# Kernel tuning notes

Hardware: AMD Instinct MI355X
Metric: run time of the kernel (lower is better)

The kernel has to match this reference:

```python
import jax, jax.numpy as jnp
import numpy as np

B, S, HID = 1, 2048, 2048
NH, NKV, HD = 32, 8, 64
INTER = 8192
EPS = 1e-6


def rmsnorm(x, w, eps=EPS):
    xf = x.astype(jnp.float32)
    inv = jax.lax.rsqrt(jnp.mean(xf * xf, axis=-1, keepdims=True) + eps)
    return (xf * inv * w).astype(x.dtype)


def rope(x, sin_t, cos_t):
    # x: [B, S, H, D]; sin/cos: [S, D//2]
    sin = sin_t[None, :, None, :]
    cos = cos_t[None, :, None, :]
    d2 = x.shape[-1] // 2
    x0, x1 = x[..., :d2], x[..., d2:]
    return jnp.concatenate((x0 * cos - x1 * sin, x0 * sin + x1 * cos), axis=-1)


def setup_inputs() -> dict:
    key = jax.random.key(0)
    ks = jax.random.split(key, 12)
    hidden_states = jax.random.normal(ks[0], (B, S, HID), dtype=jnp.float32)
    # realistic RoPE tables
    inv_freq = 1.0 / (10000.0 ** (np.arange(0, HD // 2, dtype=np.float32) * 2.0 / HD))
    ang = np.arange(S, dtype=np.float32)[:, None] * inv_freq[None, :]
    sin_table = jnp.asarray(np.sin(ang))
    cos_table = jnp.asarray(np.cos(ang))
    s = 0.02
    return {
        "hidden_states": hidden_states,
        "sin_table": sin_table,
        "cos_table": cos_table,
        "ln1_w": jnp.ones((HID,), jnp.float32),
        "ln2_w": jnp.ones((HID,), jnp.float32),
        "wq": jax.random.normal(ks[1], (HID, NH * HD), jnp.float32) * s,
        "wk": jax.random.normal(ks[2], (HID, NKV * HD), jnp.float32) * s,
        "wv": jax.random.normal(ks[3], (HID, NKV * HD), jnp.float32) * s,
        "wo": jax.random.normal(ks[4], (NH * HD, HID), jnp.float32) * s,
        "w_gate": jax.random.normal(ks[5], (HID, INTER), jnp.float32) * s,
        "w_up": jax.random.normal(ks[6], (HID, INTER), jnp.float32) * s,
        "w_down": jax.random.normal(ks[7], (INTER, HID), jnp.float32) * s,
    }


def attention(x, sin_t, cos_t, wq, wk, wv, wo):
    b, s, _ = x.shape
    q = (x @ wq).reshape(b, s, NH, HD)
    k = (x @ wk).reshape(b, s, NKV, HD)
    v = (x @ wv).reshape(b, s, NKV, HD).transpose(0, 2, 1, 3)  # [B,Hk,S,D]
    q = rope(q, sin_t, cos_t).transpose(0, 2, 1, 3)  # [B,Hq,S,D]
    k = rope(k, sin_t, cos_t).transpose(0, 2, 1, 3)  # [B,Hk,S,D]
    g = NH // NKV
    k = jnp.repeat(k, g, axis=1)
    v = jnp.repeat(v, g, axis=1)
    scale = 1.0 / np.sqrt(HD)
    scores = jnp.einsum("bhqd,bhkd->bhqk", q, k) * scale
    mask = jnp.tril(jnp.ones((s, s), dtype=bool))
    scores = jnp.where(mask, scores, -jnp.inf)
    probs = jax.nn.softmax(scores, axis=-1)
    out = jnp.einsum("bhqk,bhkd->bhqd", probs, v)
    out = out.transpose(0, 2, 1, 3).reshape(b, s, NH * HD)
    return out @ wo


def reference(hidden_states, sin_table, cos_table, ln1_w, ln2_w, wq, wk, wv, wo, w_gate, w_up, w_down):
    x = hidden_states
    x = x + attention(rmsnorm(x, ln1_w), sin_table, cos_table, wq, wk, wv, wo)
    h = rmsnorm(x, ln2_w)
    x = x + (jax.nn.silu(h @ w_gate) * (h @ w_up)) @ w_down
    return x
```

## Files before the change

kernel.cpp:

```cpp
#include <hip/hip_runtime.h>
#include <hip/hip_bf16.h>

typedef float f32x4 __attribute__((ext_vector_type(4)));
typedef unsigned int u32x4 __attribute__((ext_vector_type(4)));
typedef _Float16 f16x4 __attribute__((ext_vector_type(4)));
typedef unsigned short u16;

#define S_LEN 2048
#define HID 2048
#define NHEAD 32
#define NKVH 8
#define HDIM 64

__device__ __forceinline__ unsigned short f2bf_bits(float f) {
    unsigned int u = __builtin_bit_cast(unsigned int, f);
    unsigned int r = u + 0x7fffu + ((u >> 16) & 1u);
    return (unsigned short)(r >> 16);
}
__device__ __forceinline__ float bf2f(unsigned short b) {
    unsigned int u = ((unsigned int)b) << 16;
    return __builtin_bit_cast(float, u);
}

__device__ __forceinline__ f32x4 mfma_bf16(u32x4 a, u32x4 b, f32x4 c) {
    asm("v_mfma_f32_16x16x32_bf16 %0, %1, %2, %0" : "+v"(c) : "v"(a), "v"(b));
    return c;
}

__device__ __forceinline__ void gload_lds16(const void* g, void* l) {
    __builtin_amdgcn_global_load_lds(
        (const __attribute__((address_space(1))) void*)g,
        (__attribute__((address_space(3))) void*)l, 16, 0, 0);
}

__global__ __launch_bounds__(256)
void rmsnorm_k(const float* __restrict__ x, const float* __restrict__ wgt,
               unsigned short* __restrict__ out)
{
    int row = blockIdx.x;
    int t = threadIdx.x;
    const float* xr = x + (size_t)row * HID;
    f32x4 a = *(const f32x4*)(xr + t * 8);
    f32x4 b = *(const f32x4*)(xr + t * 8 + 4);
    float s = 0.f;
#pragma unroll
    for (int i = 0; i < 4; ++i) s += a[i] * a[i] + b[i] * b[i];
#pragma unroll
    for (int off = 32; off > 0; off >>= 1) s += __shfl_down(s, off);
    __shared__ float red[4];
    if ((t & 63) == 0) red[t >> 6] = s;
    __syncthreads();
    float tot = red[0] + red[1] + red[2] + red[3];
    float inv = rsqrtf(tot * (1.0f / (float)HID) + 1e-6f);
    f32x4 wa = *(const f32x4*)(wgt + t * 8);
    f32x4 wb = *(const f32x4*)(wgt + t * 8 + 4);
    unsigned int pk[4];
#pragma unroll
    for (int i = 0; i < 2; ++i) {
        pk[i]     = (unsigned)f2bf_bits(a[2*i] * inv * wa[2*i]) |
                    ((unsigned)f2bf_bits(a[2*i+1] * inv * wa[2*i+1]) << 16);
        pk[i + 2] = (unsigned)f2bf_bits(b[2*i] * inv * wb[2*i]) |
                    ((unsigned)f2bf_bits(b[2*i+1] * inv * wb[2*i+1]) << 16);
    }
    u32x4 ov; ov[0] = pk[0]; ov[1] = pk[1]; ov[2] = pk[2]; ov[3] = pk[3];
    *(u32x4*)(out + (size_t)row * HID + t * 8) = ov;
}

__global__ __launch_bounds__(256)
void transpose_cvt(const float* __restrict__ in, unsigned short* __restrict__ out,
                   int K, int N)
{
    __shared__ unsigned short tile[64 * 65];
    int kb = blockIdx.y * 64, nb = blockIdx.x * 64;
    int t = threadIdx.x;
    int r = t >> 2, c0 = (t & 3) * 16;
    const float* src = in + (size_t)(kb + r) * N + nb + c0;
#pragma unroll
    for (int j = 0; j < 4; ++j) {
        f32x4 v = *(const f32x4*)(src + j * 4);
#pragma unroll
        for (int i = 0; i < 4; ++i)
            tile[r * 65 + c0 + j * 4 + i] = f2bf_bits(v[i]);
    }
    __syncthreads();
    unsigned short e[16];
#pragma unroll
    for (int j = 0; j < 16; ++j) e[j] = tile[(c0 + j) * 65 + r];
    u32x4 o0, o1;
#pragma unroll
    for (int j = 0; j < 4; ++j) {
        o0[j] = (unsigned)e[2*j] | ((unsigned)e[2*j+1] << 16);
        o1[j] = (unsigned)e[8 + 2*j] | ((unsigned)e[8 + 2*j+1] << 16);
    }
    unsigned short* dst = out + (size_t)(nb + r) * K + kb + c0;
    *(u32x4*)(dst) = o0;
    *(u32x4*)(dst + 8) = o1;
}

__global__ __launch_bounds__(256)
void rope_k(unsigned short* __restrict__ qkv, const float* __restrict__ sin_t,
            const float* __restrict__ cos_t)
{
    int s = blockIdx.x;
    for (int it = threadIdx.x; it < (NHEAD + NKVH) * 32; it += 256) {
        int slot = it >> 5;
        int d = it & 31;
        int col = (slot < NHEAD) ? slot * 64 + d : HID + (slot - NHEAD) * 64 + d;
        unsigned short* p = qkv + (size_t)s * 3072 + col;
        float x0 = bf2f(p[0]);
        float x1 = bf2f(p[32]);
        float c = cos_t[s * 32 + d];
        float sn = sin_t[s * 32 + d];
        p[0]  = f2bf_bits(x0 * c - x1 * sn);
        p[32] = f2bf_bits(x0 * sn + x1 * c);
    }
}

__global__ __launch_bounds__(256)
void transpose_v(const unsigned short* __restrict__ qkv, unsigned short* __restrict__ vT)
{
    __shared__ unsigned short tile[64][80];
    int kb = blockIdx.x * 64, kvh = blockIdx.y;
    int t = threadIdx.x;
    int r = t >> 2, c0 = (t & 3) * 16;
    const unsigned short* src = qkv + (size_t)(kb + r) * 3072 + 2560 + kvh * 64 + c0;
    u32x4 v0 = *(const u32x4*)(src);
    u32x4 v1 = *(const u32x4*)(src + 8);
    *(u32x4*)&tile[r][c0] = v0;
    *(u32x4*)&tile[r][c0 + 8] = v1;
    __syncthreads();
    int d = t >> 2, k0 = (t & 3) * 16;
    unsigned short e[16];
#pragma unroll
    for (int j = 0; j < 16; ++j) e[j] = tile[k0 + j][d];
    u32x4 o0, o1;
#pragma unroll
    for (int j = 0; j < 4; ++j) {
        o0[j] = (unsigned)e[2*j] | ((unsigned)e[2*j+1] << 16);
        o1[j] = (unsigned)e[8 + 2*j] | ((unsigned)e[8 + 2*j+1] << 16);
    }
    int s0 = ((k0 >> 3) ^ (d & 7)) & 7;
    int s1 = (((k0 >> 3) + 1) ^ (d & 7)) & 7;
    unsigned short* dst = vT + ((size_t)kvh * 64 + d) * 2048 + kb;
    *(u32x4*)(dst + s0 * 8) = o0;
    *(u32x4*)(dst + s1 * 8) = o1;
}

template <int EPI>
__global__ __launch_bounds__(256)
void gemm_bt(const unsigned short* __restrict__ A,
             const unsigned short* __restrict__ Bt,
             void* __restrict__ outp, const void* __restrict__ auxp,
             int M, int N, int Kc, int lda)
{
    __shared__ unsigned short As[2][128 * 32];
    __shared__ unsigned short Bs[2][128 * 32];
    int t = threadIdx.x, w = t >> 6, l = t & 63;
    int rb = blockIdx.y, cb = blockIdx.x, zb = blockIdx.z;
    int wr = w >> 1, wc = w & 1;
    int l4 = l >> 4, l15 = l & 15;
    int arow = l >> 2, acol = (l & 3) * 8;
    f32x4 acc[4][4] = {};
    const unsigned short* Ag = A + (size_t)rb * 128 * lda + (size_t)zb * Kc
                                 + (size_t)(w * 16 + arow) * lda + acol;
    const unsigned short* Bg = Bt + (size_t)cb * 128 * lda + (size_t)zb * Kc
                                 + (size_t)(w * 16 + arow) * lda + acol;
    int nk = Kc >> 5;

#define STAGE(buf, kt)                                                          \
    {                                                                           \
        const unsigned short* Agk = Ag + (size_t)(kt) * 32;                     \
        const unsigned short* Bgk = Bg + (size_t)(kt) * 32;                     \
        gload_lds16(Agk, &As[buf][w * 512]);                                    \
        gload_lds16(Agk + (size_t)64 * lda, &As[buf][(4 + w) * 512]);           \
        gload_lds16(Bgk, &Bs[buf][w * 512]);                                    \
        gload_lds16(Bgk + (size_t)64 * lda, &Bs[buf][(4 + w) * 512]);           \
    }

    STAGE(0, 0);
    __syncthreads();
    int cur = 0;
    for (int kt = 0; kt < nk; ++kt) {
        if (kt + 1 < nk) STAGE(cur ^ 1, kt + 1);
        u32x4 af[4], bfr[4];
#pragma unroll
        for (int i = 0; i < 4; ++i)
            af[i] = *(const u32x4*)(&As[cur][(wr * 64 + i * 16 + l15) * 32 + l4 * 8]);
#pragma unroll
        for (int n = 0; n < 4; ++n)
            bfr[n] = *(const u32x4*)(&Bs[cur][(wc * 64 + n * 16 + l15) * 32 + l4 * 8]);
#pragma unroll
        for (int i = 0; i < 4; ++i)
#pragma unroll
            for (int n = 0; n < 4; ++n)
                acc[i][n] = mfma_bf16(af[i], bfr[n], acc[i][n]);
        __syncthreads();
        cur ^= 1;
    }
#undef STAGE

    int row0 = rb * 128 + wr * 64 + l4 * 4;
    int col0 = cb * 128 + wc * 64 + l15;
#pragma unroll
    for (int i = 0; i < 4; ++i) {
#pragma unroll
        for (int n = 0; n < 4; ++n) {
#pragma unroll
            for (int r = 0; r < 4; ++r) {
                int row = row0 + i * 16 + r;
                int col = col0 + n * 16;
                size_t idx = (size_t)row * N + col;
                float v = acc[i][n][r];
                if (EPI == 0) {
                    ((unsigned short*)outp)[idx] = f2bf_bits(v);
                } else if (EPI == 3) {
                    ((float*)outp)[idx] = v + ((const float*)auxp)[idx];
                } else {
                    ((_Float16*)outp)[(size_t)zb * M * N + idx] = (_Float16)v;
                }
            }
        }
    }
}

template <int KK, int QUAD, int WAITN>
__device__ __forceinline__ void phase8(u16* lds, int cur, f32x4 (&acc)[8][4],
                                       u32x4 (&bfv)[4],
                                       int aoff, int boff,
                                       const u16* Asrc, const u16* Bsrc,
                                       int K, int kt_next, bool dostage,
                                       int dst0, int dst1)
{
    const u16* ah = lds + (cur * 4 + KK * 2) * 8192 + aoff + QUAD * 2048;
    u32x4 af[4];
#pragma unroll
    for (int mi = 0; mi < 4; ++mi) af[mi] = *(const u32x4*)(ah + mi * 512);
    if (QUAD == 0) {
        const u16* bh = lds + (cur * 4 + KK * 2 + 1) * 8192 + boff;
#pragma unroll
        for (int ni = 0; ni < 4; ++ni) bfv[ni] = *(const u32x4*)(bh + ni * 512);
    }
    if (dostage) {
        const u16* src = (QUAD ? Bsrc : Asrc) + (size_t)kt_next * 64 + KK * 32;
        u16* d = lds + ((cur ^ 1) * 4 + (KK * 2 + QUAD)) * 8192;
        gload_lds16(src, d + dst0);
        gload_lds16(src + (size_t)128 * K, d + dst1);
    }
    __builtin_amdgcn_s_barrier();
    asm volatile("s_waitcnt lgkmcnt(0)" ::: "memory");
    __builtin_amdgcn_sched_barrier(0);
    __builtin_amdgcn_s_setprio(1);
#pragma unroll
    for (int mi = 0; mi < 4; ++mi)
#pragma unroll
        for (int ni = 0; ni < 4; ++ni)
            acc[QUAD * 4 + mi][ni] = mfma_bf16(af[mi], bfv[ni], acc[QUAD * 4 + mi][ni]);
    __builtin_amdgcn_s_setprio(0);
    if (WAITN == 4) asm volatile("s_waitcnt vmcnt(4)" ::: "memory");
    else if (WAITN == 0) asm volatile("s_waitcnt vmcnt(0)" ::: "memory");
    __builtin_amdgcn_s_barrier();
}

template <int EPI>
__global__ __launch_bounds__(512, 2)
void gemm8p(const u16* __restrict__ A, const u16* __restrict__ Bt,
            void* __restrict__ outp, const void* __restrict__ auxp,
            int M, int N, int K)
{
    extern __shared__ u16 lds[];
    const int tid = threadIdx.x;
    const int w = tid >> 6, l = tid & 63;
    const int wm = w >> 2, wn = w & 3;
    const int l4 = l >> 4, l15 = l & 15;

    int wg = blockIdx.x, nwg = gridDim.x;
    int swzb = ((nwg & 7) == 0) ? ((wg & 7) * (nwg >> 3) + (wg >> 3)) : wg;
    int rbs = M >> 8;
    int rb = swzb % rbs, cb = swzb / rbs;

    const int sw = ((tid & 3) ^ ((tid >> 3) & 3)) * 8;
    const int srow = tid >> 2;
    const u16* Asrc = A + (size_t)(rb * 256 + srow) * K + sw;
    const u16* Bsrc = Bt + (size_t)(cb * 256 + srow) * K + sw;
    const int dst0 = tid * 8, dst1 = (512 + tid) * 8;

    const int rswz = (l15 >> 1) & 3;
    const int aoff = (wm * 128 + l15) * 32 + (l4 ^ rswz) * 8;
    const int boff = (wn * 64 + l15) * 32 + (l4 ^ rswz) * 8;

    f32x4 acc[8][4] = {};
    u32x4 bfv[4];
    const int NT = K >> 6;

#pragma unroll
    for (int h = 0; h < 2; ++h) {
        const u16* sA = Asrc + h * 32;
        const u16* sB = Bsrc + h * 32;
        gload_lds16(sA, lds + (h * 2) * 8192 + dst0);
        gload_lds16(sA + (size_t)128 * K, lds + (h * 2) * 8192 + dst1);
        gload_lds16(sB, lds + (h * 2 + 1) * 8192 + dst0);
        gload_lds16(sB + (size_t)128 * K, lds + (h * 2 + 1) * 8192 + dst1);
    }
    asm volatile("s_waitcnt vmcnt(4)" ::: "memory");
    __builtin_amdgcn_s_barrier();

    for (int t = 0; t < NT - 1; ++t) {
        int cur = t & 1;
        phase8<0, 0, -1>(lds, cur, acc, bfv, aoff, boff, Asrc, Bsrc, K, t + 1, true, dst0, dst1);
        phase8<0, 1,  4>(lds, cur, acc, bfv, aoff, boff, Asrc, Bsrc, K, t + 1, true, dst0, dst1);
        phase8<1, 0, -1>(lds, cur, acc, bfv, aoff, boff, Asrc, Bsrc, K, t + 1, true, dst0, dst1);
        phase8<1, 1,  4>(lds, cur, acc, bfv, aoff, boff, Asrc, Bsrc, K, t + 1, true, dst0, dst1);
    }
    {
        int cur = (NT - 1) & 1;
        phase8<0, 0, -1>(lds, cur, acc, bfv, aoff, boff, Asrc, Bsrc, K, 0, false, dst0, dst1);
        phase8<0, 1,  0>(lds, cur, acc, bfv, aoff, boff, Asrc, Bsrc, K, 0, false, dst0, dst1);
        phase8<1, 0, -1>(lds, cur, acc, bfv, aoff, boff, Asrc, Bsrc, K, 0, false, dst0, dst1);
        phase8<1, 1, -1>(lds, cur, acc, bfv, aoff, boff, Asrc, Bsrc, K, 0, false, dst0, dst1);
    }

    int row0 = rb * 256 + wm * 128 + l4 * 4;
    int col0 = cb * 256 + wn * 64 + l15;
#pragma unroll
    for (int mi = 0; mi < 8; ++mi) {
#pragma unroll
        for (int ni = 0; ni < 4; ++ni) {
#pragma unroll
            for (int r = 0; r < 4; ++r) {
                int row = row0 + mi * 16 + r;
                int col = col0 + ni * 16;
                size_t idx = (size_t)row * N + col;
                float v = acc[mi][ni][r];
                if (EPI == 1) {
                    float sv = v / (1.0f + __expf(-v));
                    ((unsigned short*)outp)[idx] = f2bf_bits(sv);
                } else {
                    float gv = bf2f(((const unsigned short*)auxp)[idx]);
                    ((unsigned short*)outp)[idx] = f2bf_bits(v * gv);
                }
            }
        }
    }
}

__global__ __launch_bounds__(256)
void reduce_add4(float* __restrict__ out, const _Float16* __restrict__ p, int n)
{
    int i = (blockIdx.x * 256 + threadIdx.x) * 4;
    f32x4 a = *(const f32x4*)(out + i);
#pragma unroll
    for (int z = 0; z < 4; ++z) {
        f16x4 h = *(const f16x4*)(p + (size_t)z * n + i);
#pragma unroll
        for (int j = 0; j < 4; ++j) a[j] += (float)h[j];
    }
    *(f32x4*)(out + i) = a;
}

__global__ __launch_bounds__(256)
void attn_fwd(const unsigned short* __restrict__ qkv,
              const unsigned short* __restrict__ vT,
              unsigned short* __restrict__ out)
{
    int p = blockIdx.x, h = blockIdx.y, kvh = h >> 2;
    int t = threadIdx.x, w = t >> 6, l = t & 63;
    int l4 = l >> 4, l15 = l & 15;
    __shared__ unsigned short Ks[2][64 * 64];
    __shared__ unsigned short Vs[2][64 * 64];
    __shared__ unsigned short Pl[4][16 * 72];
    unsigned short* Pw = &Pl[w][0];

    const unsigned short* Kg = qkv + HID + kvh * 64;
    const unsigned short* Vg = vT + (size_t)kvh * 64 * 2048;

    int ch0 = w * 2, ch1 = w * 2 + 1;
    int rsub = l >> 3;
    int ksw = ((l & 7) ^ (rsub & 7)) * 8;
    int vcol = (l & 7) * 8;
    int sw0 = (l4 ^ (l15 & 7)) * 8;
    int sw1 = ((l4 | 4) ^ (l15 & 7)) * 8;

#define STAGE_KV(buf, kt)                                                         \
    {                                                                             \
        gload_lds16(Kg + (size_t)((kt) * 64 + ch0 * 8 + rsub) * 3072 + ksw,       \
                    &Ks[buf][ch0 * 512]);                                         \
        gload_lds16(Kg + (size_t)((kt) * 64 + ch1 * 8 + rsub) * 3072 + ksw,       \
                    &Ks[buf][ch1 * 512]);                                         \
        gload_lds16(Vg + (size_t)(ch0 * 8 + rsub) * 2048 + (kt) * 64 + vcol,      \
                    &Vs[buf][ch0 * 512]);                                         \
        gload_lds16(Vg + (size_t)(ch1 * 8 + rsub) * 2048 + (kt) * 64 + vcol,      \
                    &Vs[buf][ch1 * 512]);                                         \
    }

    const float SC2 = 0.18033688f;
    const float THR = 44.36f;
    const float BIG = -3.0e38f;

    for (int half = 0; half < 2; ++half) {
        int qb = half ? (31 - p) : p;
        int qrow0 = qb * 64 + w * 16;
        STAGE_KV(0, 0);
        const unsigned short* qg = qkv + (size_t)(qrow0 + l15) * 3072 + h * 64 + l4 * 8;
        u32x4 aq0 = *(const u32x4*)(qg);
        u32x4 aq1 = *(const u32x4*)(qg + 32);
        f32x4 o[4] = {};
        float m[4], ls[4] = {};
#pragma unroll
        for (int r = 0; r < 4; ++r) m[r] = BIG;
        __syncthreads();
        int cur = 0;
        for (int kt = 0; kt <= qb; ++kt) {
            if (kt < qb) STAGE_KV(cur ^ 1, kt + 1);
            f32x4 sc[4];
#pragma unroll
            for (int n = 0; n < 4; ++n) {
                const unsigned short* kb_ = &Ks[cur][(n * 16 + l15) * 64];
                u32x4 b0 = *(const u32x4*)(kb_ + sw0);
                u32x4 b1 = *(const u32x4*)(kb_ + sw1);
                f32x4 z = {};
                z = mfma_bf16(aq0, b0, z);
                z = mfma_bf16(aq1, b1, z);
                sc[n] = z;
            }
            if (kt == qb) {
#pragma unroll
                for (int n = 0; n < 4; ++n) {
                    int kcol = n * 16 + l15;
#pragma unroll
                    for (int r = 0; r < 4; ++r) {
                        int qr = w * 16 + l4 * 4 + r;
                        if (kcol > qr) sc[n][r] = BIG;
                    }
                }
            }
            float rmax[4];
#pragma unroll
            for (int r = 0; r < 4; ++r)
                rmax[r] = fmaxf(fmaxf(sc[0][r], sc[1][r]), fmaxf(sc[2][r], sc[3][r]));
#pragma unroll
            for (int msk = 1; msk <= 8; msk <<= 1)
#pragma unroll
                for (int r = 0; r < 4; ++r)
                    rmax[r] = fmaxf(rmax[r], __shfl_xor(rmax[r], msk));
            float need = 0.f;
#pragma unroll
            for (int r = 0; r < 4; ++r) need = fmaxf(need, rmax[r] - m[r]);
            if (__ballot(need > THR)) {
#pragma unroll
                for (int r = 0; r < 4; ++r) {
                    float mn = fmaxf(m[r], rmax[r]);
                    float al = __builtin_exp2f((m[r] - mn) * SC2);
                    m[r] = mn;
                    ls[r] *= al;
#pragma unroll
                    for (int nd = 0; nd < 4; ++nd) o[nd][r] *= al;
                }
            }
            float rs[4] = {}, ms[4];
#pragma unroll
            for (int r = 0; r < 4; ++r) ms[r] = m[r] * SC2;
#pragma unroll
            for (int n = 0; n < 4; ++n)
#pragma unroll
                for (int r = 0; r < 4; ++r) {
                    float pe = __builtin_exp2f(__builtin_fmaf(sc[n][r], SC2, -ms[r]));
                    sc[n][r] = pe;
                    rs[r] += pe;
                }
#pragma unroll
            for (int msk = 1; msk <= 8; msk <<= 1)
#pragma unroll
                for (int r = 0; r < 4; ++r) rs[r] += __shfl_xor(rs[r], msk);
#pragma unroll
            for (int r = 0; r < 4; ++r) ls[r] += rs[r];
#pragma unroll
            for (int n = 0; n < 4; ++n)
#pragma unroll
                for (int r = 0; r < 4; ++r)
                    Pw[(l4 * 4 + r) * 72 + n * 16 + l15] = f2bf_bits(sc[n][r]);
            asm volatile("s_waitcnt lgkmcnt(0)" ::: "memory");
            __builtin_amdgcn_sched_barrier(0);
            u32x4 ap0 = *(const u32x4*)(Pw + l15 * 72 + l4 * 8);
            u32x4 ap1 = *(const u32x4*)(Pw + l15 * 72 + 32 + l4 * 8);
#pragma unroll
            for (int nd = 0; nd < 4; ++nd) {
                const unsigned short* vb = &Vs[cur][(nd * 16 + l15) * 64];
                u32x4 bv0 = *(const u32x4*)(vb + sw0);
                u32x4 bv1 = *(const u32x4*)(vb + sw1);
                o[nd] = mfma_bf16(ap0, bv0, o[nd]);
                o[nd] = mfma_bf16(ap1, bv1, o[nd]);
            }
            __syncthreads();
            cur ^= 1;
        }
#undef STAGE_KV
        float linv[4];
#pragma unroll
        for (int r = 0; r < 4; ++r) linv[r] = 1.0f / ls[r];
#pragma unroll
        for (int nd = 0; nd < 4; ++nd)
#pragma unroll
            for (int r = 0; r < 4; ++r)
                out[(size_t)(qrow0 + l4 * 4 + r) * HID + h * 64 + nd * 16 + l15] =
                    f2bf_bits(o[nd][r] * linv[r]);
    }
}

extern "C" void kernel_launch(void* const* d_in, const int* in_sizes, int n_in,
                              void* d_out, int out_size, void* d_ws, size_t ws_size,
                              hipStream_t stream)
{
    const float* x     = (const float*)d_in[0];
    const float* sin_t = (const float*)d_in[1];
    const float* cos_t = (const float*)d_in[2];
    const float* ln1w  = (const float*)d_in[3];
    const float* ln2w  = (const float*)d_in[4];
    const float* wq    = (const float*)d_in[5];
    const float* wk    = (const float*)d_in[6];
    const float* wv    = (const float*)d_in[7];
    const float* wo    = (const float*)d_in[8];
    const float* wg    = (const float*)d_in[9];
    const float* wu    = (const float*)d_in[10];
    const float* wd    = (const float*)d_in[11];
    float* out = (float*)d_out;

    char* ws = (char*)d_ws;
    if (ws_size < 113246208u) return;
    unsigned short* wT   = (unsigned short*)(ws);
    unsigned short* xn   = (unsigned short*)(ws + 33554432u);
    unsigned short* qkv  = (unsigned short*)(ws + 41943040u);
    unsigned short* attn = (unsigned short*)(ws + 54525952u);
    unsigned short* vT   = (unsigned short*)(ws + 62914560u);
    _Float16*       part = (_Float16*)(ws + 33554432u);
    unsigned short* g    = (unsigned short*)(ws + 79691776u);

    hipFuncSetAttribute(reinterpret_cast<const void*>(&gemm8p<1>),
                        hipFuncAttributeMaxDynamicSharedMemorySize, 131072);
    hipFuncSetAttribute(reinterpret_cast<const void*>(&gemm8p<2>),
                        hipFuncAttributeMaxDynamicSharedMemorySize, 131072);

    rmsnorm_k<<<S_LEN, 256, 0, stream>>>(x, ln1w, xn);

    transpose_cvt<<<dim3(32, 32), 256, 0, stream>>>(wq, wT, 2048, 2048);
    transpose_cvt<<<dim3(8, 32), 256, 0, stream>>>(wk, wT + (size_t)2048 * 2048, 2048, 512);
    transpose_cvt<<<dim3(8, 32), 256, 0, stream>>>(wv, wT + (size_t)2560 * 2048, 2048, 512);

    gemm_bt<0><<<dim3(24, 16, 1), 256, 0, stream>>>(xn, wT, qkv, nullptr, 2048, 3072, 2048, 2048);

    rope_k<<<S_LEN, 256, 0, stream>>>(qkv, sin_t, cos_t);
    transpose_v<<<dim3(32, 8), 256, 0, stream>>>(qkv, vT);

    attn_fwd<<<dim3(16, 32), 256, 0, stream>>>(qkv, vT, attn);

    transpose_cvt<<<dim3(32, 32), 256, 0, stream>>>(wo, wT, 2048, 2048);
    gemm_bt<3><<<dim3(16, 16, 1), 256, 0, stream>>>(attn, wT, out, x, 2048, 2048, 2048, 2048);

    rmsnorm_k<<<S_LEN, 256, 0, stream>>>(out, ln2w, xn);

    transpose_cvt<<<dim3(128, 32), 256, 0, stream>>>(wg, wT, 2048, 8192);
    gemm8p<1><<<dim3(256), 512, 131072, stream>>>(xn, wT, g, nullptr, 2048, 8192, 2048);

    transpose_cvt<<<dim3(128, 32), 256, 0, stream>>>(wu, wT, 2048, 8192);
    gemm8p<2><<<dim3(256), 512, 131072, stream>>>(xn, wT, g, g, 2048, 8192, 2048);

    transpose_cvt<<<dim3(32, 128), 256, 0, stream>>>(wd, wT, 8192, 2048);
    gemm_bt<5><<<dim3(16, 16, 4), 256, 0, stream>>>(g, wT, part, nullptr, 2048, 2048, 2048, 8192);

    reduce_add4<<<4096, 256, 0, stream>>>(out, part, 4194304);
}
```

Baseline: 485.2 us.

## Use split-K 256x256 gemm8p for down-proj and split-K the o-proj

Extends the pipelined 256x256 gemm8p kernel with split-K support: a separate leading dimension, a K-chunk offset taken from blockIdx.y, and an fp16 partial-output epilogue. The down projection now runs on gemm8p (64 tiles x 4 K-splits) in place of the smaller-tile gemm_bt, aiming at higher MFMA efficiency. The o-projection is split into two K halves writing fp16 partials, followed by a new reduce kernel that adds the residual, so the grid has more blocks. The cost is an extra reduction kernel and fp16 rounding of the partial sums.

```diff
diff --git a/kernel.cpp b/kernel.cpp
--- a/kernel.cpp
+++ b/kernel.cpp
@@ -228,7 +228,7 @@
                                        u32x4 (&bfv)[4],
                                        int aoff, int boff,
                                        const u16* Asrc, const u16* Bsrc,
-                                       int K, int kt_next, bool dostage,
+                                       int lda, int kt_next, bool dostage,
                                        int dst0, int dst1)
 {
     const u16* ah = lds + (cur * 4 + KK * 2) * 8192 + aoff + QUAD * 2048;
@@ -244,7 +244,7 @@
         const u16* src = (QUAD ? Bsrc : Asrc) + (size_t)kt_next * 64 + KK * 32;
         u16* d = lds + ((cur ^ 1) * 4 + (KK * 2 + QUAD)) * 8192;
         gload_lds16(src, d + dst0);
-        gload_lds16(src + (size_t)128 * K, d + dst1);
+        gload_lds16(src + (size_t)128 * lda, d + dst1);
     }
     __builtin_amdgcn_s_barrier();
     asm volatile("s_waitcnt lgkmcnt(0)" ::: "memory");
@@ -265,13 +265,14 @@
 __global__ __launch_bounds__(512, 2)
 void gemm8p(const u16* __restrict__ A, const u16* __restrict__ Bt,
             void* __restrict__ outp, const void* __restrict__ auxp,
-            int M, int N, int K)
+            int M, int N, int Kc, int lda)
 {
     extern __shared__ u16 lds[];
     const int tid = threadIdx.x;
     const int w = tid >> 6, l = tid & 63;
     const int wm = w >> 2, wn = w & 3;
     const int l4 = l >> 4, l15 = l & 15;
+    const int zb = blockIdx.y;
 
     int wg = blockIdx.x, nwg = gridDim.x;
     int swzb = ((nwg & 7) == 0) ? ((wg & 7) * (nwg >> 3) + (wg >> 3)) : wg;
@@ -280,8 +281,8 @@
 
     const int sw = ((tid & 3) ^ ((tid >> 3) & 3)) * 8;
     const int srow = tid >> 2;
-    const u16* Asrc = A + (size_t)(rb * 256 + srow) * K + sw;
-    const u16* Bsrc = Bt + (size_t)(cb * 256 + srow) * K + sw;
+    const u16* Asrc = A + (size_t)(rb * 256 + srow) * lda + (size_t)zb * Kc + sw;
+    const u16* Bsrc = Bt + (size_t)(cb * 256 + srow) * lda + (size_t)zb * Kc + sw;
     const int dst0 = tid * 8, dst1 = (512 + tid) * 8;
 
     const int rswz = (l15 >> 1) & 3;
@@ -290,33 +291,33 @@
 
     f32x4 acc[8][4] = {};
     u32x4 bfv[4];
-    const int NT = K >> 6;
+    const int NT = Kc >> 6;
 
 #pragma unroll
     for (int h = 0; h < 2; ++h) {
         const u16* sA = Asrc + h * 32;
         const u16* sB = Bsrc + h * 32;
         gload_lds16(sA, lds + (h * 2) * 8192 + dst0);
-        gload_lds16(sA + (size_t)128 * K, lds + (h * 2) * 8192 + dst1);
+        gload_lds16(sA + (size_t)128 * lda, lds + (h * 2) * 8192 + dst1);
         gload_lds16(sB, lds + (h * 2 + 1) * 8192 + dst0);
-        gload_lds16(sB + (size_t)128 * K, lds + (h * 2 + 1) * 8192 + dst1);
+        gload_lds16(sB + (size_t)128 * lda, lds + (h * 2 + 1) * 8192 + dst1);
     }
     asm volatile("s_waitcnt vmcnt(4)" ::: "memory");
     __builtin_amdgcn_s_barrier();
 
     for (int t = 0; t < NT - 1; ++t) {
         int cur = t & 1;
-        phase8<0, 0, -1>(lds, cur, acc, bfv, aoff, boff, Asrc, Bsrc, K, t + 1, true, dst0, dst1);
-        phase8<0, 1,  4>(lds, cur, acc, bfv, aoff, boff, Asrc, Bsrc, K, t + 1, true, dst0, dst1);
-        phase8<1, 0, -1>(lds, cur, acc, bfv, aoff, boff, Asrc, Bsrc, K, t + 1, true, dst0, dst1);
-        phase8<1, 1,  4>(lds, cur, acc, bfv, aoff, boff, Asrc, Bsrc, K, t + 1, true, dst0, dst1);
+        phase8<0, 0, -1>(lds, cur, acc, bfv, aoff, boff, Asrc, Bsrc, lda, t + 1, true, dst0, dst1);
+        phase8<0, 1,  4>(lds, cur, acc, bfv, aoff, boff, Asrc, Bsrc, lda, t + 1, true, dst0, dst1);
+        phase8<1, 0, -1>(lds, cur, acc, bfv, aoff, boff, Asrc, Bsrc, lda, t + 1, true, dst0, dst1);
+        phase8<1, 1,  4>(lds, cur, acc, bfv, aoff, boff, Asrc, Bsrc, lda, t + 1, true, dst0, dst1);
     }
     {
         int cur = (NT - 1) & 1;
-        phase8<0, 0, -1>(lds, cur, acc, bfv, aoff, boff, Asrc, Bsrc, K, 0, false, dst0, dst1);
-        phase8<0, 1,  0>(lds, cur, acc, bfv, aoff, boff, Asrc, Bsrc, K, 0, false, dst0, dst1);
-        phase8<1, 0, -1>(lds, cur, acc, bfv, aoff, boff, Asrc, Bsrc, K, 0, false, dst0, dst1);
-        phase8<1, 1, -1>(lds, cur, acc, bfv, aoff, boff, Asrc, Bsrc, K, 0, false, dst0, dst1);
+        phase8<0, 0, -1>(lds, cur, acc, bfv, aoff, boff, Asrc, Bsrc, lda, 0, false, dst0, dst1);
+        phase8<0, 1,  0>(lds, cur, acc, bfv, aoff, boff, Asrc, Bsrc, lda, 0, false, dst0, dst1);
+        phase8<1, 0, -1>(lds, cur, acc, bfv, aoff, boff, Asrc, Bsrc, lda, 0, false, dst0, dst1);
+        phase8<1, 1, -1>(lds, cur, acc, bfv, aoff, boff, Asrc, Bsrc, lda, 0, false, dst0, dst1);
     }
 
     int row0 = rb * 256 + wm * 128 + l4 * 4;
@@ -334,9 +335,11 @@
                 if (EPI == 1) {
                     float sv = v / (1.0f + __expf(-v));
                     ((unsigned short*)outp)[idx] = f2bf_bits(sv);
-                } else {
+                } else if (EPI == 2) {
                     float gv = bf2f(((const unsigned short*)auxp)[idx]);
                     ((unsigned short*)outp)[idx] = f2bf_bits(v * gv);
+                } else {
+                    ((_Float16*)outp)[(size_t)zb * M * N + idx] = (_Float16)v;
                 }
             }
         }
@@ -350,6 +353,21 @@
     f32x4 a = *(const f32x4*)(out + i);
 #pragma unroll
     for (int z = 0; z < 4; ++z) {
+        f16x4 h = *(const f16x4*)(p + (size_t)z * n + i);
+#pragma unroll
+        for (int j = 0; j < 4; ++j) a[j] += (float)h[j];
+    }
+    *(f32x4*)(out + i) = a;
+}
+
+__global__ __launch_bounds__(256)
+void reduce_res2(float* __restrict__ out, const float* __restrict__ x,
+                 const _Float16* __restrict__ p, int n)
+{
+    int i = (blockIdx.x * 256 + threadIdx.x) * 4;
+    f32x4 a = *(const f32x4*)(x + i);
+#pragma unroll
+    for (int z = 0; z < 2; ++z) {
         f16x4 h = *(const f16x4*)(p + (size_t)z * n + i);
 #pragma unroll
         for (int j = 0; j < 4; ++j) a[j] += (float)h[j];
@@ -533,11 +551,14 @@
     unsigned short* vT   = (unsigned short*)(ws + 62914560u);
     _Float16*       part = (_Float16*)(ws + 33554432u);
     unsigned short* g    = (unsigned short*)(ws + 79691776u);
+    _Float16*       opart = (_Float16*)(ws + 79691776u);
 
     hipFuncSetAttribute(reinterpret_cast<const void*>(&gemm8p<1>),
                         hipFuncAttributeMaxDynamicSharedMemorySize, 131072);
     hipFuncSetAttribute(reinterpret_cast<const void*>(&gemm8p<2>),
                         hipFuncAttributeMaxDynamicSharedMemorySize, 131072);
+    hipFuncSetAttribute(reinterpret_cast<const void*>(&gemm8p<5>),
+                        hipFuncAttributeMaxDynamicSharedMemorySize, 131072);
 
     rmsnorm_k<<<S_LEN, 256, 0, stream>>>(x, ln1w, xn);
 
@@ -553,18 +574,19 @@
     attn_fwd<<<dim3(16, 32), 256, 0, stream>>>(qkv, vT, attn);
 
     transpose_cvt<<<dim3(32, 32), 256, 0, stream>>>(wo, wT, 2048, 2048);
-    gemm_bt<3><<<dim3(16, 16, 1), 256, 0, stream>>>(attn, wT, out, x, 2048, 2048, 2048, 2048);
+    gemm_bt<5><<<dim3(16, 16, 2), 256, 0, stream>>>(attn, wT, opart, nullptr, 2048, 2048, 1024, 2048);
+    reduce_res2<<<4096, 256, 0, stream>>>(out, x, opart, 4194304);
 
     rmsnorm_k<<<S_LEN, 256, 0, stream>>>(out, ln2w, xn);
 
     transpose_cvt<<<dim3(128, 32), 256, 0, stream>>>(wg, wT, 2048, 8192);
-    gemm8p<1><<<dim3(256), 512, 131072, stream>>>(xn, wT, g, nullptr, 2048, 8192, 2048);
+    gemm8p<1><<<dim3(256, 1), 512, 131072, stream>>>(xn, wT, g, nullptr, 2048, 8192, 2048, 2048);
 
     transpose_cvt<<<dim3(128, 32), 256, 0, stream>>>(wu, wT, 2048, 8192);
-    gemm8p<2><<<dim3(256), 512, 131072, stream>>>(xn, wT, g, g, 2048, 8192, 2048);
+    gemm8p<2><<<dim3(256, 1), 512, 131072, stream>>>(xn, wT, g, g, 2048, 8192, 2048, 2048);
 
     transpose_cvt<<<dim3(32, 128), 256, 0, stream>>>(wd, wT, 8192, 2048);
-    gemm_bt<5><<<dim3(16, 16, 4), 256, 0, stream>>>(g, wT, part, nullptr, 2048, 2048, 2048, 8192);
+    gemm8p<5><<<dim3(64, 4), 512, 131072, stream>>>(g, wT, part, nullptr, 2048, 2048, 2048, 8192);
 
     reduce_add4<<<4096, 256, 0, stream>>>(out, part, 4194304);
 }
```

New measurement: 465.3 us. 1.04x faster.
